# Kernel optimization log

Hardware: AMD Instinct MI355X
Metric: run time of the kernel (lower is better)

The kernel has to match this reference:

```python
import jax, jax.numpy as jnp
import numpy as np

TOTAL_WORDS = 10000
EMB = 100
SEQ = 80
UNITS = 64
BATCH = 8192


def setup_inputs() -> dict:
    key = jax.random.key(0)
    ks = jax.random.split(key, 10)
    sc = 0.05
    return {
        "tokens": jax.random.randint(ks[0], (BATCH, SEQ), 0, TOTAL_WORDS, dtype=jnp.int32),
        "emb": jax.random.normal(ks[1], (TOTAL_WORDS, EMB), jnp.float32) * sc,
        "W1x": jax.random.normal(ks[2], (EMB, UNITS), jnp.float32) * sc,
        "W1h": jax.random.normal(ks[3], (UNITS, UNITS), jnp.float32) * sc,
        "b1": jnp.zeros((UNITS,), jnp.float32),
        "W2x": jax.random.normal(ks[4], (UNITS, UNITS), jnp.float32) * sc,
        "W2h": jax.random.normal(ks[5], (UNITS, UNITS), jnp.float32) * sc,
        "b2": jnp.zeros((UNITS,), jnp.float32),
        "Wd": jax.random.normal(ks[6], (UNITS, 1), jnp.float32) * sc,
        "bd": jnp.zeros((1,), jnp.float32),
    }


def _simple_rnn(x, Wx, Wh, b):
    # x: [B, T, D] -> all hidden states [B, T, H] (Keras SimpleRNN, tanh)
    B = x.shape[0]
    H = Wh.shape[0]
    h0 = jnp.zeros((B, H), x.dtype)

    def step(h, xt):
        h = jnp.tanh(xt @ Wx + h @ Wh + b)
        return h, h

    _, hs = jax.lax.scan(step, h0, jnp.swapaxes(x, 0, 1))  # hs: [T, B, H]
    return jnp.swapaxes(hs, 0, 1)


def reference(tokens, emb, W1x, W1h, b1, W2x, W2h, b2, Wd, bd):
    x = emb[tokens]                      # [B, T, EMB] embedding lookup
    h1 = _simple_rnn(x, W1x, W1h, b1)    # [B, T, U] return_sequences=True
    h2 = _simple_rnn(h1, W2x, W2h, b2)[:, -1, :]  # last state, [B, U]
    logits = h2 @ Wd + bd                # [B, 1]
    return jax.nn.sigmoid(logits)
```

## Files before the change

### kernel.cpp

```cpp
#include <hip/hip_runtime.h>
#include <hip/hip_bf16.h>

#define TOTALW 10000
#define BATCH 8192
#define SEQ   80
#define EMBD  100
#define UNITS 64
#define MB    16
#define NTHREADS 256
#define HPAD  80
#define TOKPAD 84

typedef __attribute__((ext_vector_type(8))) _Float16 half8;
typedef __attribute__((ext_vector_type(2))) _Float16 half2v;
typedef __attribute__((ext_vector_type(4))) float floatx4;

__device__ __forceinline__ half2v pkh(float a, float b) {
#if __has_builtin(__builtin_amdgcn_cvt_pkrtz)
  return (half2v)__builtin_amdgcn_cvt_pkrtz(a, b);
#else
  return half2v{(_Float16)a, (_Float16)b};
#endif
}
__device__ __forceinline__ int h2i(half2v h) {
  union { half2v h; int i; } c; c.h = h; return c.i;
}
__device__ __forceinline__ half2v pk_tanh(half2v x) {
  const half2v c3 = {(_Float16)-0.0359280f, (_Float16)-0.0359280f};
  const half2v c2 = {(_Float16) 0.1270784f, (_Float16) 0.1270784f};
  const half2v c1 = {(_Float16)-0.3324617f, (_Float16)-0.3324617f};
  const half2v c0 = {(_Float16) 0.9999660f, (_Float16) 0.9999660f};
  const half2v t = x * x;
  half2v p = __builtin_elementwise_fma(c3, t, c2);
  p = __builtin_elementwise_fma(p, t, c1);
  p = __builtin_elementwise_fma(p, t, c0);
  return x * p;
}

__launch_bounds__(256)
__global__ void emb_proj_mfma(const float* __restrict__ emb,
                              const float* __restrict__ W1x,
                              const float* __restrict__ b1,
                              float* __restrict__ xw) {
  __shared__ __align__(16) _Float16 Es[16][128];
  const int tid  = threadIdx.x;
  const int wave = tid >> 6;
  const int lane = tid & 63;
  const int li   = lane & 15;
  const int quad = lane >> 4;
  const int q4   = quad * 4;

  half8 bw[4];
  #pragma unroll
  for (int kc = 0; kc < 4; ++kc) {
    half8 f;
    #pragma unroll
    for (int j = 0; j < 8; ++j) {
      const int k = kc * 32 + quad * 8 + j;
      f[j] = (k < EMBD) ? (_Float16)W1x[k * UNITS + wave * 16 + li] : (_Float16)0.0f;
    }
    bw[kc] = f;
  }
  const float bb = b1[wave * 16 + li];

  for (int task = tid; task < 16 * 14; task += 256) {
    const int r = task / 14, c = task % 14;
    *(int*)(&Es[r][100 + c * 2]) = 0;
  }

  for (int rowBase = blockIdx.x * 16; rowBase < TOTALW; rowBase += 512 * 16) {
    __syncthreads();
    for (int task = tid; task < 16 * 25; task += 256) {
      const int r = task / 25, c = task % 25;
      const float4 v = *(const float4*)(emb + (rowBase + r) * EMBD + c * 4);
      *(int2*)(&Es[r][c * 4]) = make_int2(h2i(pkh(v.x, v.y)), h2i(pkh(v.z, v.w)));
    }
    __syncthreads();
    floatx4 acc = {bb, bb, bb, bb};
    #pragma unroll
    for (int kc = 0; kc < 4; ++kc) {
      const half8 a = *(const half8*)(&Es[li][kc * 32 + quad * 8]);
      acc = __builtin_amdgcn_mfma_f32_16x16x32_f16(a, bw[kc], acc, 0, 0, 0);
    }
    #pragma unroll
    for (int i = 0; i < 4; ++i)
      xw[(rowBase + q4 + i) * UNITS + wave * 16 + li] = acc[i];
  }
}

__launch_bounds__(NTHREADS, 2)
__global__ void rnn2_kernel(const int* __restrict__ tokens,
                            const float* __restrict__ xw,
                            const float* __restrict__ W1h,
                            const float* __restrict__ W2x,
                            const float* __restrict__ W2h,
                            const float* __restrict__ b2,
                            const float* __restrict__ Wd,
                            const float* __restrict__ bd,
                            float* __restrict__ out)
{
  __shared__ __align__(16) _Float16 H1s[2][MB][HPAD];
  __shared__ __align__(16) _Float16 H2s[2][MB][HPAD];
  __shared__ __align__(16) int      tok[MB][TOKPAD];

  const int tid  = threadIdx.x;
  const int wave = tid >> 6;
  const int lane = tid & 63;
  const int li   = lane & 15;
  const int quad = lane >> 4;
  const int u     = wave * 16 + li;
  const int ubase = wave * 16 + quad * 4;
  const int rowBase = blockIdx.x * MB;

  for (int task = tid; task < MB * 20; task += NTHREADS) {
    const int r = task / 20, c = task % 20;
    *(int4*)(&tok[r][c * 4]) = *(const int4*)(tokens + (rowBase + r) * SEQ + c * 4);
  }
  for (int task = tid; task < MB * 4; task += NTHREADS)
    tok[task >> 2][SEQ + (task & 3)] = 0;
  for (int i = tid; i < MB * HPAD / 2; i += NTHREADS)
    ((int*)&H2s[1][0][0])[i] = 0;

  half8 w1h[2], w2x[2], w2h[2];
  #pragma unroll
  for (int kc = 0; kc < 2; ++kc) {
    half8 f, g, h;
    #pragma unroll
    for (int j = 0; j < 8; ++j) {
      const int k = kc * 32 + quad * 8 + j;
      f[j] = (_Float16)W1h[k * UNITS + u];
      g[j] = (_Float16)W2x[k * UNITS + u];
      h[j] = (_Float16)W2h[k * UNITS + u];
    }
    w1h[kc] = f; w2x[kc] = g; w2h[kc] = h;
  }
  const float4 b2f = *(const float4*)(b2 + ubase);

  float4 wdv[4];
  float  bdv = 0.f;
  if (wave == 0) {
    const int s = lane & 3;
    #pragma unroll
    for (int i = 0; i < 4; ++i)
      wdv[i] = *(const float4*)(Wd + s * 16 + i * 4);
    bdv = bd[0];
  }

  __syncthreads();

  float4 xw0, xw1;
  {
    const int tk0 = tok[li][0];
    const float4 x0 = *(const float4*)(xw + tk0 * UNITS + ubase);
    *(int2*)(&H1s[0][li][ubase]) = make_int2(h2i(pk_tanh(pkh(x0.x, x0.y))),
                                             h2i(pk_tanh(pkh(x0.z, x0.w))));
    const int tk1 = tok[li][1];
    xw0 = *(const float4*)(xw + tk1 * UNITS + ubase);
  }
  int tkA = tok[li][2];
  int tkB = tok[li][3];
  __syncthreads();

#define STEP(T, CUR, NXT, TKU, PF, XWC, XWN)                                    \
  {                                                                             \
    if (PF) {                                                                   \
      XWN = *(const float4*)(xw + (TKU) * UNITS + ubase);                       \
      TKU = tok[li][(T) + 4];                                                   \
    }                                                                           \
    const half8 h1a0 = *(const half8*)(&H1s[CUR][li][quad * 8]);                \
    const half8 h1a1 = *(const half8*)(&H1s[CUR][li][32 + quad * 8]);           \
    const half8 h2a0 = *(const half8*)(&H2s[NXT][li][quad * 8]);                \
    const half8 h2a1 = *(const half8*)(&H2s[NXT][li][32 + quad * 8]);           \
    floatx4 accA = {b2f.x, b2f.y, b2f.z, b2f.w};                                \
    floatx4 accB = {0.f, 0.f, 0.f, 0.f};                                        \
    accA = __builtin_amdgcn_mfma_f32_16x16x32_f16(w2x[0], h1a0, accA, 0, 0, 0); \
    accB = __builtin_amdgcn_mfma_f32_16x16x32_f16(w2h[0], h2a0, accB, 0, 0, 0); \
    accA = __builtin_amdgcn_mfma_f32_16x16x32_f16(w2x[1], h1a1, accA, 0, 0, 0); \
    accB = __builtin_amdgcn_mfma_f32_16x16x32_f16(w2h[1], h2a1, accB, 0, 0, 0); \
    floatx4 acc1 = {(XWC).x, (XWC).y, (XWC).z, (XWC).w};                        \
    acc1 = __builtin_amdgcn_mfma_f32_16x16x32_f16(w1h[0], h1a0, acc1, 0, 0, 0); \
    acc1 = __builtin_amdgcn_mfma_f32_16x16x32_f16(w1h[1], h1a1, acc1, 0, 0, 0); \
    const half2v s0 = pk_tanh(pkh(accA[0] + accB[0], accA[1] + accB[1]));       \
    const half2v s1 = pk_tanh(pkh(accA[2] + accB[2], accA[3] + accB[3]));       \
    *(int2*)(&H2s[CUR][li][ubase]) = make_int2(h2i(s0), h2i(s1));               \
    const half2v c0 = pk_tanh(pkh(acc1[0], acc1[1]));                           \
    const half2v c1 = pk_tanh(pkh(acc1[2], acc1[3]));                           \
    *(int2*)(&H1s[NXT][li][ubase]) = make_int2(h2i(c0), h2i(c1));               \
    __syncthreads();                                                            \
  }

  for (int t = 0; t < SEQ - 2; t += 2) {
    STEP(t,     0, 1, tkA, 1, xw0, xw1)
    STEP(t + 1, 1, 0, tkB, 1, xw1, xw0)
  }
  STEP(SEQ - 2, 0, 1, tkA, 0, xw0, xw1)

  {
    const half8 h1a0 = *(const half8*)(&H1s[1][li][quad * 8]);
    const half8 h1a1 = *(const half8*)(&H1s[1][li][32 + quad * 8]);
    const half8 h2a0 = *(const half8*)(&H2s[0][li][quad * 8]);
    const half8 h2a1 = *(const half8*)(&H2s[0][li][32 + quad * 8]);
    floatx4 accA = {b2f.x, b2f.y, b2f.z, b2f.w};
    floatx4 accB = {0.f, 0.f, 0.f, 0.f};
    accA = __builtin_amdgcn_mfma_f32_16x16x32_f16(w2x[0], h1a0, accA, 0, 0, 0);
    accB = __builtin_amdgcn_mfma_f32_16x16x32_f16(w2h[0], h2a0, accB, 0, 0, 0);
    accA = __builtin_amdgcn_mfma_f32_16x16x32_f16(w2x[1], h1a1, accA, 0, 0, 0);
    accB = __builtin_amdgcn_mfma_f32_16x16x32_f16(w2h[1], h2a1, accB, 0, 0, 0);
    const half2v s0 = pk_tanh(pkh(accA[0] + accB[0], accA[1] + accB[1]));
    const half2v s1 = pk_tanh(pkh(accA[2] + accB[2], accA[3] + accB[3]));
    *(int2*)(&H2s[1][li][ubase]) = make_int2(h2i(s0), h2i(s1));
  }
  __syncthreads();

  if (wave == 0) {
    const int r = lane >> 2, s = lane & 3;
    const _Float16* hrow = &H2s[1][r][0];
    float acc = 0.f;
    #pragma unroll
    for (int i = 0; i < 4; ++i) {
      const int base = s * 16 + i * 4;
      acc += (float)hrow[base + 0] * wdv[i].x + (float)hrow[base + 1] * wdv[i].y
           + (float)hrow[base + 2] * wdv[i].z + (float)hrow[base + 3] * wdv[i].w;
    }
    acc += __shfl_xor(acc, 1);
    acc += __shfl_xor(acc, 2);
    if (s == 0) out[rowBase + r] = 1.0f / (1.0f + __expf(-(acc + bdv)));
  }
#undef STEP
}

extern "C" void kernel_launch(void* const* d_in, const int* in_sizes, int n_in,
                              void* d_out, int out_size, void* d_ws, size_t ws_size,
                              hipStream_t stream) {
  const int*   tokens = (const int*)d_in[0];
  const float* emb    = (const float*)d_in[1];
  const float* W1x    = (const float*)d_in[2];
  const float* W1h    = (const float*)d_in[3];
  const float* b1     = (const float*)d_in[4];
  const float* W2x    = (const float*)d_in[5];
  const float* W2h    = (const float*)d_in[6];
  const float* b2     = (const float*)d_in[7];
  const float* Wd     = (const float*)d_in[8];
  const float* bd     = (const float*)d_in[9];
  float* out = (float*)d_out;
  float* xw  = (float*)d_ws;

  emb_proj_mfma<<<512, 256, 0, stream>>>(emb, W1x, b1, xw);
  rnn2_kernel<<<BATCH / MB, NTHREADS, 0, stream>>>(tokens, xw, W1h, W2x, W2h,
                                                   b2, Wd, bd, out);
}
```

Before: 106.6 us.

## Store projected embedding table in fp16 and add it after recurrent MFMA

The precomputed embedding-times-W1x table is now written as fp16 instead of fp32, halving the bytes gathered per token in the recurrent kernel. The projection kernel launches one block per 16-row tile instead of a grid-stride loop, with swapped MFMA operands so each lane writes four contiguous units as packed halves. In the recurrence the x-projection is no longer the MFMA accumulator seed; it is added in fp16 after the recurrent MFMA. This loses some precision in the layer-1 pre-activation sum.

```diff
diff --git a/kernel.cpp b/kernel.cpp
--- a/kernel.cpp
+++ b/kernel.cpp
@@ -24,6 +24,9 @@
 }
 __device__ __forceinline__ int h2i(half2v h) {
   union { half2v h; int i; } c; c.h = h; return c.i;
+}
+__device__ __forceinline__ half2v i2h(int i) {
+  union { int i; half2v h; } c; c.i = i; return c.h;
 }
 __device__ __forceinline__ half2v pk_tanh(half2v x) {
   const half2v c3 = {(_Float16)-0.0359280f, (_Float16)-0.0359280f};
@@ -41,16 +44,25 @@
 __global__ void emb_proj_mfma(const float* __restrict__ emb,
                               const float* __restrict__ W1x,
                               const float* __restrict__ b1,
-                              float* __restrict__ xw) {
+                              _Float16* __restrict__ xw) {
   __shared__ __align__(16) _Float16 Es[16][128];
   const int tid  = threadIdx.x;
   const int wave = tid >> 6;
   const int lane = tid & 63;
   const int li   = lane & 15;
   const int quad = lane >> 4;
-  const int q4   = quad * 4;
-
-  half8 bw[4];
+  const int rowBase = blockIdx.x * 16;
+
+  for (int task = tid; task < 16 * 25; task += 256) {
+    const int r = task / 25, c = task % 25;
+    const float4 v = *(const float4*)(emb + (rowBase + r) * EMBD + c * 4);
+    *(int2*)(&Es[r][c * 4]) = make_int2(h2i(pkh(v.x, v.y)), h2i(pkh(v.z, v.w)));
+  }
+  for (int task = tid; task < 16 * 14; task += 256) {
+    const int r = task / 14, c = task % 14;
+    *(int*)(&Es[r][100 + c * 2]) = 0;
+  }
+  half8 aw[4];
   #pragma unroll
   for (int kc = 0; kc < 4; ++kc) {
     half8 f;
@@ -59,38 +71,26 @@
       const int k = kc * 32 + quad * 8 + j;
       f[j] = (k < EMBD) ? (_Float16)W1x[k * UNITS + wave * 16 + li] : (_Float16)0.0f;
     }
-    bw[kc] = f;
-  }
-  const float bb = b1[wave * 16 + li];
-
-  for (int task = tid; task < 16 * 14; task += 256) {
-    const int r = task / 14, c = task % 14;
-    *(int*)(&Es[r][100 + c * 2]) = 0;
-  }
-
-  for (int rowBase = blockIdx.x * 16; rowBase < TOTALW; rowBase += 512 * 16) {
-    __syncthreads();
-    for (int task = tid; task < 16 * 25; task += 256) {
-      const int r = task / 25, c = task % 25;
-      const float4 v = *(const float4*)(emb + (rowBase + r) * EMBD + c * 4);
-      *(int2*)(&Es[r][c * 4]) = make_int2(h2i(pkh(v.x, v.y)), h2i(pkh(v.z, v.w)));
-    }
-    __syncthreads();
-    floatx4 acc = {bb, bb, bb, bb};
-    #pragma unroll
-    for (int kc = 0; kc < 4; ++kc) {
-      const half8 a = *(const half8*)(&Es[li][kc * 32 + quad * 8]);
-      acc = __builtin_amdgcn_mfma_f32_16x16x32_f16(a, bw[kc], acc, 0, 0, 0);
-    }
-    #pragma unroll
-    for (int i = 0; i < 4; ++i)
-      xw[(rowBase + q4 + i) * UNITS + wave * 16 + li] = acc[i];
-  }
+    aw[kc] = f;
+  }
+  const float4 b1v = *(const float4*)(b1 + wave * 16 + quad * 4);
+  __syncthreads();
+
+  floatx4 acc = {b1v.x, b1v.y, b1v.z, b1v.w};
+  #pragma unroll
+  for (int kc = 0; kc < 4; ++kc) {
+    const half8 b = *(const half8*)(&Es[li][kc * 32 + quad * 8]);
+    acc = __builtin_amdgcn_mfma_f32_16x16x32_f16(aw[kc], b, acc, 0, 0, 0);
+  }
+  const half2v p0 = pkh(acc[0], acc[1]);
+  const half2v p1 = pkh(acc[2], acc[3]);
+  *(int2*)(xw + (rowBase + li) * UNITS + wave * 16 + quad * 4) =
+      make_int2(h2i(p0), h2i(p1));
 }
 
 __launch_bounds__(NTHREADS, 2)
 __global__ void rnn2_kernel(const int* __restrict__ tokens,
-                            const float* __restrict__ xw,
+                            const _Float16* __restrict__ xw,
                             const float* __restrict__ W1h,
                             const float* __restrict__ W2x,
                             const float* __restrict__ W2h,
@@ -148,14 +148,14 @@
 
   __syncthreads();
 
-  float4 xw0, xw1;
+  int2 xw0, xw1;
   {
     const int tk0 = tok[li][0];
-    const float4 x0 = *(const float4*)(xw + tk0 * UNITS + ubase);
-    *(int2*)(&H1s[0][li][ubase]) = make_int2(h2i(pk_tanh(pkh(x0.x, x0.y))),
-                                             h2i(pk_tanh(pkh(x0.z, x0.w))));
+    const int2 x0 = *(const int2*)(xw + tk0 * UNITS + ubase);
+    *(int2*)(&H1s[0][li][ubase]) = make_int2(h2i(pk_tanh(i2h(x0.x))),
+                                             h2i(pk_tanh(i2h(x0.y))));
     const int tk1 = tok[li][1];
-    xw0 = *(const float4*)(xw + tk1 * UNITS + ubase);
+    xw0 = *(const int2*)(xw + tk1 * UNITS + ubase);
   }
   int tkA = tok[li][2];
   int tkB = tok[li][3];
@@ -164,7 +164,7 @@
 #define STEP(T, CUR, NXT, TKU, PF, XWC, XWN)                                    \
   {                                                                             \
     if (PF) {                                                                   \
-      XWN = *(const float4*)(xw + (TKU) * UNITS + ubase);                       \
+      XWN = *(const int2*)(xw + (TKU) * UNITS + ubase);                         \
       TKU = tok[li][(T) + 4];                                                   \
     }                                                                           \
     const half8 h1a0 = *(const half8*)(&H1s[CUR][li][quad * 8]);                \
@@ -173,18 +173,18 @@
     const half8 h2a1 = *(const half8*)(&H2s[NXT][li][32 + quad * 8]);           \
     floatx4 accA = {b2f.x, b2f.y, b2f.z, b2f.w};                                \
     floatx4 accB = {0.f, 0.f, 0.f, 0.f};                                        \
+    floatx4 acc1 = {0.f, 0.f, 0.f, 0.f};                                        \
     accA = __builtin_amdgcn_mfma_f32_16x16x32_f16(w2x[0], h1a0, accA, 0, 0, 0); \
     accB = __builtin_amdgcn_mfma_f32_16x16x32_f16(w2h[0], h2a0, accB, 0, 0, 0); \
     accA = __builtin_amdgcn_mfma_f32_16x16x32_f16(w2x[1], h1a1, accA, 0, 0, 0); \
     accB = __builtin_amdgcn_mfma_f32_16x16x32_f16(w2h[1], h2a1, accB, 0, 0, 0); \
-    floatx4 acc1 = {(XWC).x, (XWC).y, (XWC).z, (XWC).w};                        \
     acc1 = __builtin_amdgcn_mfma_f32_16x16x32_f16(w1h[0], h1a0, acc1, 0, 0, 0); \
     acc1 = __builtin_amdgcn_mfma_f32_16x16x32_f16(w1h[1], h1a1, acc1, 0, 0, 0); \
     const half2v s0 = pk_tanh(pkh(accA[0] + accB[0], accA[1] + accB[1]));       \
     const half2v s1 = pk_tanh(pkh(accA[2] + accB[2], accA[3] + accB[3]));       \
     *(int2*)(&H2s[CUR][li][ubase]) = make_int2(h2i(s0), h2i(s1));               \
-    const half2v c0 = pk_tanh(pkh(acc1[0], acc1[1]));                           \
-    const half2v c1 = pk_tanh(pkh(acc1[2], acc1[3]));                           \
+    const half2v c0 = pk_tanh(i2h((XWC).x) + pkh(acc1[0], acc1[1]));            \
+    const half2v c1 = pk_tanh(i2h((XWC).y) + pkh(acc1[2], acc1[3]));            \
     *(int2*)(&H1s[NXT][li][ubase]) = make_int2(h2i(c0), h2i(c1));               \
     __syncthreads();                                                            \
   }
@@ -243,9 +243,9 @@
   const float* Wd     = (const float*)d_in[8];
   const float* bd     = (const float*)d_in[9];
   float* out = (float*)d_out;
-  float* xw  = (float*)d_ws;
-
-  emb_proj_mfma<<<512, 256, 0, stream>>>(emb, W1x, b1, xw);
+  _Float16* xw = (_Float16*)d_ws;
+
+  emb_proj_mfma<<<TOTALW / 16, 256, 0, stream>>>(emb, W1x, b1, xw);
   rnn2_kernel<<<BATCH / MB, NTHREADS, 0, stream>>>(tokens, xw, W1h, W2x, W2h,
                                                    b2, Wd, bd, out);
 }
```

New measurement: 103.7 us (median of 2 runs). 1.03x faster.
